# Performance work log

Measured on AMD Instinct MI355X. Metric: run time of the kernel, lower is better.

## Reference

```python
import jax, jax.numpy as jnp
import numpy as np

HEADS = 8
DIM_HEAD = 64


def setup_inputs() -> dict:
    key = jax.random.key(0)
    ks = jax.random.split(key, 8)
    B, L, m = 4, 1024, 64
    Dq, Dc = 512, 256
    inner = HEADS * DIM_HEAD  # 512
    x = jax.random.normal(ks[0], (B, L, Dq), dtype=jnp.float32)
    context = jax.random.normal(ks[1], (B, L, m, Dc), dtype=jnp.float32)
    mask = jax.random.randint(ks[2], (B, L, m), 0, 2).astype(bool)
    # guarantee at least one valid token per (b,l) row
    mask = mask.at[:, :, 0].set(True)
    bias = jax.random.normal(ks[3], (B, L, m), dtype=jnp.float32)
    s = 0.02
    Wq = jax.random.normal(ks[4], (Dq, inner), dtype=jnp.float32) * s
    Wk = jax.random.normal(ks[5], (Dc, inner), dtype=jnp.float32) * s
    Wv = jax.random.normal(ks[6], (Dc, inner), dtype=jnp.float32) * s
    Wo = jax.random.normal(ks[7], (inner, Dq), dtype=jnp.float32) * s
    bo = jnp.zeros((Dq,), dtype=jnp.float32)
    return {"x": x, "context": context, "mask": mask, "bias": bias,
            "Wq": Wq, "Wk": Wk, "Wv": Wv, "Wo": Wo, "bo": bo}


def reference(x, context, mask, bias, Wq, Wk, Wv, Wo, bo):
    B, L, Dq = x.shape
    m = context.shape[2]
    scale = DIM_HEAD ** (-0.5)
    # projections
    Q = (x @ Wq).reshape(B, L, HEADS, DIM_HEAD)                 # b l h d
    K = (context @ Wk).reshape(B, L, m, HEADS, DIM_HEAD)        # b l m h d
    V = (context @ Wv).reshape(B, L, m, HEADS, DIM_HEAD)        # b l m h d
    scores = jnp.einsum('blhd,blmhd->blhm', Q, K) * scale       # b l h m
    scores = scores + bias[:, :, None, :]
    scores = jnp.where(mask[:, :, None, :], scores, -jnp.inf)
    attn = jax.nn.softmax(scores, axis=-1)
    out = jnp.einsum('blhm,blmhd->blhd', attn, V).reshape(B, L, HEADS * DIM_HEAD)
    return out @ Wo + bo
```

## Files before the change

kernel.cpp:

```cpp
#include <hip/hip_runtime.h>
#include <cstddef>


typedef __attribute__((ext_vector_type(8))) short short8;
typedef __attribute__((ext_vector_type(4))) float float4v;

__device__ __forceinline__ short f2bf(float f) {
  unsigned u = __float_as_uint(f);
  return (short)((u + 0x7fffu + ((u >> 16) & 1u)) >> 16);
}

__global__ __launch_bounds__(256) void k_cvt(const float* __restrict__ x,
                                             const float* __restrict__ Wk,
                                             const float* __restrict__ Wv,
                                             short* __restrict__ xb,
                                             short* __restrict__ Wkb,
                                             short* __restrict__ Wvb) {
  size_t i4 = ((size_t)blockIdx.x * 256 + threadIdx.x) * 4;
  const float* src; short* dst; size_t off;
  if (i4 < 2097152)       { src = x;  dst = xb;  off = i4; }
  else if (i4 < 2228224)  { src = Wk; dst = Wkb; off = i4 - 2097152; }
  else                    { src = Wv; dst = Wvb; off = i4 - 2228224; }
  float4 v = *(const float4*)(src + off);
  short4 o; o.x = f2bf(v.x); o.y = f2bf(v.y); o.z = f2bf(v.z); o.w = f2bf(v.w);
  *(short4*)(dst + off) = o;
}

__global__ __launch_bounds__(256) void k_tcvt(const float* __restrict__ in,
                                              short* __restrict__ out) {
  int id = blockIdx.x * 256 + threadIdx.x;
  int k = id >> 9, n = id & 511;
  out[(size_t)n * 512 + k] = f2bf(in[(size_t)k * 512 + n]);
}

__global__ __launch_bounds__(256) void k_mm(const short* __restrict__ A,
                                            const short* __restrict__ Bt,
                                            const float* __restrict__ bias,
                                            void* __restrict__ C,
                                            int lda, int ldb, int ldc, int K,
                                            int bShift, int bMask, int bHS, int crossAK,
                                            float scale, int storeBF16) {
  __shared__ short As[128 * 72];
  __shared__ short Bs[128 * 72];
  int t = threadIdx.x;
  int n0 = blockIdx.x * 128, m0 = blockIdx.y * 128;
  int hb = n0 >> bShift;
  const short* aBase = A + (size_t)m0 * lda + (size_t)hb * crossAK;
  const short* bBase = Bt + (size_t)(n0 & bMask) * ldb + (size_t)hb * bHS;
  int w = t >> 6, l = t & 63;
  int wm = w & 1, wn = w >> 1;
  int li = l & 15, kq = l >> 4;
  float4v acc[4][4];
#pragma unroll
  for (int i = 0; i < 4; ++i)
#pragma unroll
    for (int j = 0; j < 4; ++j) acc[i][j] = (float4v){0.f, 0.f, 0.f, 0.f};

  for (int k0 = 0; k0 < K; k0 += 64) {
    __syncthreads();
#pragma unroll
    for (int p = 0; p < 4; ++p) {
      int i = p * 256 + t, row = i >> 3, kq8 = i & 7;
      *(uint4*)&As[row * 72 + kq8 * 8] = *(const uint4*)(aBase + (size_t)row * lda + k0 + kq8 * 8);
      *(uint4*)&Bs[row * 72 + kq8 * 8] = *(const uint4*)(bBase + (size_t)row * ldb + k0 + kq8 * 8);
    }
    __syncthreads();
#pragma unroll
    for (int kk = 0; kk < 2; ++kk) {
      short8 af[4], bfr[4];
#pragma unroll
      for (int i = 0; i < 4; ++i) {
        af[i]  = *(const short8*)&As[(wm * 64 + i * 16 + li) * 72 + kk * 32 + kq * 8];
        bfr[i] = *(const short8*)&Bs[(wn * 64 + i * 16 + li) * 72 + kk * 32 + kq * 8];
      }
#pragma unroll
      for (int mi = 0; mi < 4; ++mi)
#pragma unroll
        for (int ni = 0; ni < 4; ++ni)
          acc[mi][ni] = __builtin_amdgcn_mfma_f32_16x16x32_bf16(af[mi], bfr[ni], acc[mi][ni], 0, 0, 0);
    }
  }
#pragma unroll
  for (int ni = 0; ni < 4; ++ni) {
    int col = n0 + wn * 64 + ni * 16 + li;
    float bv = bias ? bias[col] : 0.f;
#pragma unroll
    for (int mi = 0; mi < 4; ++mi)
#pragma unroll
      for (int r = 0; r < 4; ++r) {
        int row = m0 + wm * 64 + mi * 16 + kq * 4 + r;
        float v = fmaf(acc[mi][ni][r], scale, bv);
        if (storeBF16) ((short*)C)[(size_t)row * ldc + col] = f2bf(v);
        else           ((float*)C)[(size_t)row * ldc + col] = v;
      }
  }
}

__global__ __launch_bounds__(256) void k_attn(const float* __restrict__ ctx,
                                              const float* __restrict__ Qk,
                                              const float* __restrict__ bias,
                                              const int* __restrict__ mask,
                                              short* __restrict__ CA) {
  __shared__ float ctxs[64 * 132];
  __shared__ float qks[2048];
  __shared__ float sc[512];
  __shared__ float bs[64];
  __shared__ int   ms[64];
  int t = threadIdx.x;
  int r = blockIdx.x;
  const float* ctxr = ctx + (size_t)r * 16384;

  const float4* q4 = (const float4*)(Qk + (size_t)r * 2048);
  ((float4*)qks)[t]       = q4[t];
  ((float4*)qks)[t + 256] = q4[t + 256];
  if (t < 64) { bs[t] = bias[(size_t)r * 64 + t]; ms[t] = mask[(size_t)r * 64 + t]; }

  int m_ = t & 63, h0 = t >> 6;
  float s0 = 0.f, s1 = 0.f;
  for (int kk = 0; kk < 2; ++kk) {
    __syncthreads();
#pragma unroll
    for (int i = 0; i < 8; ++i) {
      int l = t + i * 256;
      int m = l >> 5, c4 = l & 31;
      float4 v = *(const float4*)(ctxr + m * 256 + kk * 128 + c4 * 4);
      *(float4*)(ctxs + m * 132 + c4 * 4) = v;
    }
    __syncthreads();
    const float* cp = ctxs + m_ * 132;
    const float* q0 = qks + h0 * 256 + kk * 128;
    const float* q1 = q0 + 1024;
#pragma unroll 8
    for (int c4 = 0; c4 < 32; ++c4) {
      float4 cv = *(const float4*)(cp + c4 * 4);
      float4 qa = *(const float4*)(q0 + c4 * 4);
      float4 qb = *(const float4*)(q1 + c4 * 4);
      s0 = fmaf(cv.x, qa.x, s0); s0 = fmaf(cv.y, qa.y, s0);
      s0 = fmaf(cv.z, qa.z, s0); s0 = fmaf(cv.w, qa.w, s0);
      s1 = fmaf(cv.x, qb.x, s1); s1 = fmaf(cv.y, qb.y, s1);
      s1 = fmaf(cv.z, qb.z, s1); s1 = fmaf(cv.w, qb.w, s1);
    }
  }
  bool valid = ms[m_] != 0;
  float b = bs[m_];
  s0 = valid ? s0 + b : -INFINITY;
  s1 = valid ? s1 + b : -INFINITY;
  float mx0 = s0, mx1 = s1;
#pragma unroll
  for (int o = 32; o > 0; o >>= 1) {
    mx0 = fmaxf(mx0, __shfl_xor(mx0, o, 64));
    mx1 = fmaxf(mx1, __shfl_xor(mx1, o, 64));
  }
  float e0 = __expf(s0 - mx0), e1 = __expf(s1 - mx1);
  float sm0 = e0, sm1 = e1;
#pragma unroll
  for (int o = 32; o > 0; o >>= 1) {
    sm0 += __shfl_xor(sm0, o, 64);
    sm1 += __shfl_xor(sm1, o, 64);
  }
  sc[m_ * 8 + h0]     = e0 / sm0;
  sc[m_ * 8 + h0 + 4] = e1 / sm1;
  __syncthreads();
  float acc[8] = {};
#pragma unroll 4
  for (int m = 0; m < 64; ++m) {
    float cv = ctxr[m * 256 + t];
    float4 w0 = *(const float4*)&sc[m * 8];
    float4 w1 = *(const float4*)&sc[m * 8 + 4];
    acc[0] = fmaf(w0.x, cv, acc[0]); acc[1] = fmaf(w0.y, cv, acc[1]);
    acc[2] = fmaf(w0.z, cv, acc[2]); acc[3] = fmaf(w0.w, cv, acc[3]);
    acc[4] = fmaf(w1.x, cv, acc[4]); acc[5] = fmaf(w1.y, cv, acc[5]);
    acc[6] = fmaf(w1.z, cv, acc[6]); acc[7] = fmaf(w1.w, cv, acc[7]);
  }
  short* car = CA + (size_t)r * 2048;
#pragma unroll
  for (int hh = 0; hh < 8; ++hh) car[hh * 256 + t] = f2bf(acc[hh]);
}

extern "C" void kernel_launch(void* const* d_in, const int* in_sizes, int n_in,
                              void* d_out, int out_size, void* d_ws, size_t ws_size,
                              hipStream_t stream) {
  const float* x    = (const float*)d_in[0];
  const float* ctx  = (const float*)d_in[1];
  const int*   mask = (const int*)d_in[2];
  const float* bias = (const float*)d_in[3];
  const float* Wq   = (const float*)d_in[4];
  const float* Wk   = (const float*)d_in[5];
  const float* Wv   = (const float*)d_in[6];
  const float* Wo   = (const float*)d_in[7];
  const float* bo   = (const float*)d_in[8];
  float* out = (float*)d_out;

  char* ws = (char*)d_ws;
  short* xb    = (short*)(ws);
  short* Qb    = (short*)(ws + (4u << 20));
  float* Qk    = (float*)(ws + (8u << 20));
  short* CAb   = (short*)(ws + (40u << 20));
  short* WqTb  = (short*)(ws + (56u << 20));
  short* WoTb  = (short*)(ws + (56u << 20) + (512u << 10));
  short* Wkb   = (short*)(ws + (57u << 20));
  short* Wvb   = (short*)(ws + (57u << 20) + (256u << 10));
  short* WvoTb = (short*)(ws + (58u << 20));

  hipLaunchKernelGGL(k_cvt,  dim3(2304), dim3(256), 0, stream, x, Wk, Wv, xb, Wkb, Wvb);
  hipLaunchKernelGGL(k_tcvt, dim3(1024), dim3(256), 0, stream, Wq, WqTb);
  hipLaunchKernelGGL(k_tcvt, dim3(1024), dim3(256), 0, stream, Wo, WoTb);
  hipLaunchKernelGGL(k_mm, dim3(16, 4), dim3(256), 0, stream,
                     WoTb, Wvb, (const float*)nullptr, WvoTb,
                     512, 512, 2048, 64, 8, 255, 64, 64, 1.0f, 1);
  hipLaunchKernelGGL(k_mm, dim3(4, 32), dim3(256), 0, stream,
                     xb, WqTb, (const float*)nullptr, Qb,
                     512, 512, 512, 512, 31, 0x7fffffff, 0, 0, 1.0f, 1);
  hipLaunchKernelGGL(k_mm, dim3(16, 32), dim3(256), 0, stream,
                     Qb, Wkb, (const float*)nullptr, Qk,
                     512, 512, 2048, 64, 8, 255, 64, 64, 0.125f, 0);
  hipLaunchKernelGGL(k_attn, dim3(4096), dim3(256), 0, stream, ctx, Qk, bias, mask, CAb);
  hipLaunchKernelGGL(k_mm, dim3(4, 32), dim3(256), 0, stream,
                     CAb, WvoTb, bo, out,
                     2048, 2048, 512, 2048, 31, 0x7fffffff, 0, 0, 1.0f, 0);
}
```

Before: 485.3 us.

## Shrink GEMM tiles with register prefetch, store Qk as bf16, restructure score loop

The GEMM kernel moves from 128x128 to 128x64 tiles, which doubles the grid size. It also prefetches the next K-slice from global memory into registers while the current slice is being computed. The Q·Wk intermediate is now written as bf16, halving its traffic into the attention kernel. The attention score phase changes too: each wave handles a 16-wide slice of the context dimension for all 8 heads, and the partial results are reduced through shared memory. These changes trade extra LDS use and extra syncs, plus some bf16 rounding of Qk, for better occupancy and less memory traffic.

```diff
diff --git a/kernel.cpp b/kernel.cpp
--- a/kernel.cpp
+++ b/kernel.cpp
@@ -8,6 +8,9 @@
 __device__ __forceinline__ short f2bf(float f) {
   unsigned u = __float_as_uint(f);
   return (short)((u + 0x7fffu + ((u >> 16) & 1u)) >> 16);
+}
+__device__ __forceinline__ float bf2f(short s) {
+  return __uint_as_float(((unsigned)(unsigned short)s) << 16);
 }
 
 __global__ __launch_bounds__(256) void k_cvt(const float* __restrict__ x,
@@ -41,40 +44,66 @@
                                             int bShift, int bMask, int bHS, int crossAK,
                                             float scale, int storeBF16) {
   __shared__ short As[128 * 72];
-  __shared__ short Bs[128 * 72];
+  __shared__ short Bs[64 * 72];
   int t = threadIdx.x;
-  int n0 = blockIdx.x * 128, m0 = blockIdx.y * 128;
+  int n0 = blockIdx.x * 64, m0 = blockIdx.y * 128;
   int hb = n0 >> bShift;
   const short* aBase = A + (size_t)m0 * lda + (size_t)hb * crossAK;
   const short* bBase = Bt + (size_t)(n0 & bMask) * ldb + (size_t)hb * bHS;
   int w = t >> 6, l = t & 63;
-  int wm = w & 1, wn = w >> 1;
   int li = l & 15, kq = l >> 4;
-  float4v acc[4][4];
-#pragma unroll
-  for (int i = 0; i < 4; ++i)
+  float4v acc[2][4];
+#pragma unroll
+  for (int i = 0; i < 2; ++i)
 #pragma unroll
     for (int j = 0; j < 4; ++j) acc[i][j] = (float4v){0.f, 0.f, 0.f, 0.f};
-
+  uint4 pa[4], pb[2];
+#pragma unroll
+  for (int p = 0; p < 4; ++p) {
+    int i = p * 256 + t, row = i >> 3, kq8 = i & 7;
+    pa[p] = *(const uint4*)(aBase + (size_t)row * lda + kq8 * 8);
+  }
+#pragma unroll
+  for (int p = 0; p < 2; ++p) {
+    int i = p * 256 + t, row = i >> 3, kq8 = i & 7;
+    pb[p] = *(const uint4*)(bBase + (size_t)row * ldb + kq8 * 8);
+  }
   for (int k0 = 0; k0 < K; k0 += 64) {
     __syncthreads();
 #pragma unroll
     for (int p = 0; p < 4; ++p) {
       int i = p * 256 + t, row = i >> 3, kq8 = i & 7;
-      *(uint4*)&As[row * 72 + kq8 * 8] = *(const uint4*)(aBase + (size_t)row * lda + k0 + kq8 * 8);
-      *(uint4*)&Bs[row * 72 + kq8 * 8] = *(const uint4*)(bBase + (size_t)row * ldb + k0 + kq8 * 8);
-    }
-    __syncthreads();
+      *(uint4*)&As[row * 72 + kq8 * 8] = pa[p];
+    }
+#pragma unroll
+    for (int p = 0; p < 2; ++p) {
+      int i = p * 256 + t, row = i >> 3, kq8 = i & 7;
+      *(uint4*)&Bs[row * 72 + kq8 * 8] = pb[p];
+    }
+    __syncthreads();
+    if (k0 + 64 < K) {
+#pragma unroll
+      for (int p = 0; p < 4; ++p) {
+        int i = p * 256 + t, row = i >> 3, kq8 = i & 7;
+        pa[p] = *(const uint4*)(aBase + (size_t)row * lda + (k0 + 64) + kq8 * 8);
+      }
+#pragma unroll
+      for (int p = 0; p < 2; ++p) {
+        int i = p * 256 + t, row = i >> 3, kq8 = i & 7;
+        pb[p] = *(const uint4*)(bBase + (size_t)row * ldb + (k0 + 64) + kq8 * 8);
+      }
+    }
 #pragma unroll
     for (int kk = 0; kk < 2; ++kk) {
-      short8 af[4], bfr[4];
-#pragma unroll
-      for (int i = 0; i < 4; ++i) {
-        af[i]  = *(const short8*)&As[(wm * 64 + i * 16 + li) * 72 + kk * 32 + kq * 8];
-        bfr[i] = *(const short8*)&Bs[(wn * 64 + i * 16 + li) * 72 + kk * 32 + kq * 8];
-      }
-#pragma unroll
-      for (int mi = 0; mi < 4; ++mi)
+      short8 af[2], bfr[4];
+#pragma unroll
+      for (int mi = 0; mi < 2; ++mi)
+        af[mi] = *(const short8*)&As[(w * 32 + mi * 16 + li) * 72 + kk * 32 + kq * 8];
+#pragma unroll
+      for (int ni = 0; ni < 4; ++ni)
+        bfr[ni] = *(const short8*)&Bs[(ni * 16 + li) * 72 + kk * 32 + kq * 8];
+#pragma unroll
+      for (int mi = 0; mi < 2; ++mi)
 #pragma unroll
         for (int ni = 0; ni < 4; ++ni)
           acc[mi][ni] = __builtin_amdgcn_mfma_f32_16x16x32_bf16(af[mi], bfr[ni], acc[mi][ni], 0, 0, 0);
@@ -82,13 +111,13 @@
   }
 #pragma unroll
   for (int ni = 0; ni < 4; ++ni) {
-    int col = n0 + wn * 64 + ni * 16 + li;
+    int col = n0 + ni * 16 + li;
     float bv = bias ? bias[col] : 0.f;
 #pragma unroll
-    for (int mi = 0; mi < 4; ++mi)
+    for (int mi = 0; mi < 2; ++mi)
 #pragma unroll
       for (int r = 0; r < 4; ++r) {
-        int row = m0 + wm * 64 + mi * 16 + kq * 4 + r;
+        int row = m0 + w * 32 + mi * 16 + kq * 4 + r;
         float v = fmaf(acc[mi][ni][r], scale, bv);
         if (storeBF16) ((short*)C)[(size_t)row * ldc + col] = f2bf(v);
         else           ((float*)C)[(size_t)row * ldc + col] = v;
@@ -97,50 +126,69 @@
 }
 
 __global__ __launch_bounds__(256) void k_attn(const float* __restrict__ ctx,
-                                              const float* __restrict__ Qk,
+                                              const short* __restrict__ Qkb,
                                               const float* __restrict__ bias,
                                               const int* __restrict__ mask,
                                               short* __restrict__ CA) {
-  __shared__ float ctxs[64 * 132];
+  __shared__ float ctxs[64 * 68];
   __shared__ float qks[2048];
-  __shared__ float sc[512];
+  __shared__ float P[4 * 64 * 12];
+  __shared__ float sw[64 * 12];
   __shared__ float bs[64];
   __shared__ int   ms[64];
   int t = threadIdx.x;
   int r = blockIdx.x;
   const float* ctxr = ctx + (size_t)r * 16384;
 
-  const float4* q4 = (const float4*)(Qk + (size_t)r * 2048);
-  ((float4*)qks)[t]       = q4[t];
-  ((float4*)qks)[t + 256] = q4[t + 256];
+  {
+    uint4 q8 = *((const uint4*)(Qkb + (size_t)r * 2048) + t);
+    const short* qs = (const short*)&q8;
+    float4 lo, hi;
+    lo.x = bf2f(qs[0]); lo.y = bf2f(qs[1]); lo.z = bf2f(qs[2]); lo.w = bf2f(qs[3]);
+    hi.x = bf2f(qs[4]); hi.y = bf2f(qs[5]); hi.z = bf2f(qs[6]); hi.w = bf2f(qs[7]);
+    *(float4*)(qks + t * 8)     = lo;
+    *(float4*)(qks + t * 8 + 4) = hi;
+  }
   if (t < 64) { bs[t] = bias[(size_t)r * 64 + t]; ms[t] = mask[(size_t)r * 64 + t]; }
 
-  int m_ = t & 63, h0 = t >> 6;
-  float s0 = 0.f, s1 = 0.f;
-  for (int kk = 0; kk < 2; ++kk) {
-    __syncthreads();
-#pragma unroll
-    for (int i = 0; i < 8; ++i) {
-      int l = t + i * 256;
-      int m = l >> 5, c4 = l & 31;
-      float4 v = *(const float4*)(ctxr + m * 256 + kk * 128 + c4 * 4);
-      *(float4*)(ctxs + m * 132 + c4 * 4) = v;
-    }
-    __syncthreads();
-    const float* cp = ctxs + m_ * 132;
-    const float* q0 = qks + h0 * 256 + kk * 128;
-    const float* q1 = q0 + 1024;
-#pragma unroll 8
-    for (int c4 = 0; c4 < 32; ++c4) {
+  int m_ = t & 63, w = t >> 6;
+  float s[8] = {};
+  for (int kk = 0; kk < 4; ++kk) {
+    __syncthreads();
+#pragma unroll
+    for (int i = 0; i < 4; ++i) {
+      int idx = t + i * 256;
+      int mm = idx >> 4, c4 = idx & 15;
+      float4 v = *(const float4*)(ctxr + mm * 256 + kk * 64 + c4 * 4);
+      *(float4*)(ctxs + mm * 68 + c4 * 4) = v;
+    }
+    __syncthreads();
+    const float* cp = ctxs + m_ * 68 + w * 16;
+    const float* qb = qks + kk * 64 + w * 16;
+#pragma unroll
+    for (int c4 = 0; c4 < 4; ++c4) {
       float4 cv = *(const float4*)(cp + c4 * 4);
-      float4 qa = *(const float4*)(q0 + c4 * 4);
-      float4 qb = *(const float4*)(q1 + c4 * 4);
-      s0 = fmaf(cv.x, qa.x, s0); s0 = fmaf(cv.y, qa.y, s0);
-      s0 = fmaf(cv.z, qa.z, s0); s0 = fmaf(cv.w, qa.w, s0);
-      s1 = fmaf(cv.x, qb.x, s1); s1 = fmaf(cv.y, qb.y, s1);
-      s1 = fmaf(cv.z, qb.z, s1); s1 = fmaf(cv.w, qb.w, s1);
-    }
-  }
+#pragma unroll
+      for (int h = 0; h < 8; ++h) {
+        float4 q = *(const float4*)(qb + h * 256 + c4 * 4);
+        s[h] = fmaf(cv.x, q.x, fmaf(cv.y, q.y, fmaf(cv.z, q.z, fmaf(cv.w, q.w, s[h]))));
+      }
+    }
+  }
+  float* pp = P + w * 768 + m_ * 12;
+  *(float4*)(pp)     = make_float4(s[0], s[1], s[2], s[3]);
+  *(float4*)(pp + 4) = make_float4(s[4], s[5], s[6], s[7]);
+  __syncthreads();
+  {
+    int h = t & 7, mb = t >> 3;
+#pragma unroll
+    for (int j = 0; j < 2; ++j) {
+      int mm = mb + j * 32, o = mm * 12 + h;
+      sw[o] = P[o] + P[768 + o] + P[1536 + o] + P[2304 + o];
+    }
+  }
+  __syncthreads();
+  float s0 = sw[m_ * 12 + w], s1 = sw[m_ * 12 + w + 4];
   bool valid = ms[m_] != 0;
   float b = bs[m_];
   s0 = valid ? s0 + b : -INFINITY;
@@ -158,15 +206,15 @@
     sm0 += __shfl_xor(sm0, o, 64);
     sm1 += __shfl_xor(sm1, o, 64);
   }
-  sc[m_ * 8 + h0]     = e0 / sm0;
-  sc[m_ * 8 + h0 + 4] = e1 / sm1;
+  sw[m_ * 12 + w]     = e0 / sm0;
+  sw[m_ * 12 + w + 4] = e1 / sm1;
   __syncthreads();
   float acc[8] = {};
 #pragma unroll 4
   for (int m = 0; m < 64; ++m) {
     float cv = ctxr[m * 256 + t];
-    float4 w0 = *(const float4*)&sc[m * 8];
-    float4 w1 = *(const float4*)&sc[m * 8 + 4];
+    float4 w0 = *(const float4*)(sw + m * 12);
+    float4 w1 = *(const float4*)(sw + m * 12 + 4);
     acc[0] = fmaf(w0.x, cv, acc[0]); acc[1] = fmaf(w0.y, cv, acc[1]);
     acc[2] = fmaf(w0.z, cv, acc[2]); acc[3] = fmaf(w0.w, cv, acc[3]);
     acc[4] = fmaf(w1.x, cv, acc[4]); acc[5] = fmaf(w1.y, cv, acc[5]);
@@ -194,28 +242,28 @@
   char* ws = (char*)d_ws;
   short* xb    = (short*)(ws);
   short* Qb    = (short*)(ws + (4u << 20));
-  float* Qk    = (float*)(ws + (8u << 20));
-  short* CAb   = (short*)(ws + (40u << 20));
-  short* WqTb  = (short*)(ws + (56u << 20));
-  short* WoTb  = (short*)(ws + (56u << 20) + (512u << 10));
-  short* Wkb   = (short*)(ws + (57u << 20));
-  short* Wvb   = (short*)(ws + (57u << 20) + (256u << 10));
-  short* WvoTb = (short*)(ws + (58u << 20));
+  short* Qkb   = (short*)(ws + (8u << 20));
+  short* CAb   = (short*)(ws + (24u << 20));
+  short* WqTb  = (short*)(ws + (40u << 20));
+  short* WoTb  = (short*)(ws + (40u << 20) + (512u << 10));
+  short* Wkb   = (short*)(ws + (41u << 20));
+  short* Wvb   = (short*)(ws + (41u << 20) + (256u << 10));
+  short* WvoTb = (short*)(ws + (42u << 20));
 
   hipLaunchKernelGGL(k_cvt,  dim3(2304), dim3(256), 0, stream, x, Wk, Wv, xb, Wkb, Wvb);
   hipLaunchKernelGGL(k_tcvt, dim3(1024), dim3(256), 0, stream, Wq, WqTb);
   hipLaunchKernelGGL(k_tcvt, dim3(1024), dim3(256), 0, stream, Wo, WoTb);
-  hipLaunchKernelGGL(k_mm, dim3(16, 4), dim3(256), 0, stream,
+  hipLaunchKernelGGL(k_mm, dim3(32, 4), dim3(256), 0, stream,
                      WoTb, Wvb, (const float*)nullptr, WvoTb,
                      512, 512, 2048, 64, 8, 255, 64, 64, 1.0f, 1);
-  hipLaunchKernelGGL(k_mm, dim3(4, 32), dim3(256), 0, stream,
+  hipLaunchKernelGGL(k_mm, dim3(8, 32), dim3(256), 0, stream,
                      xb, WqTb, (const float*)nullptr, Qb,
                      512, 512, 512, 512, 31, 0x7fffffff, 0, 0, 1.0f, 1);
-  hipLaunchKernelGGL(k_mm, dim3(16, 32), dim3(256), 0, stream,
-                     Qb, Wkb, (const float*)nullptr, Qk,
-                     512, 512, 2048, 64, 8, 255, 64, 64, 0.125f, 0);
-  hipLaunchKernelGGL(k_attn, dim3(4096), dim3(256), 0, stream, ctx, Qk, bias, mask, CAb);
-  hipLaunchKernelGGL(k_mm, dim3(4, 32), dim3(256), 0, stream,
+  hipLaunchKernelGGL(k_mm, dim3(32, 32), dim3(256), 0, stream,
+                     Qb, Wkb, (const float*)nullptr, Qkb,
+                     512, 512, 2048, 64, 8, 255, 64, 64, 0.125f, 1);
+  hipLaunchKernelGGL(k_attn, dim3(4096), dim3(256), 0, stream, ctx, Qkb, bias, mask, CAb);
+  hipLaunchKernelGGL(k_mm, dim3(8, 32), dim3(256), 0, stream,
                      CAb, WvoTb, bo, out,
                      2048, 2048, 512, 2048, 31, 0x7fffffff, 0, 0, 1.0f, 0);
 }
```

After: 522.8 us. 1.08x slower.
